# Performance work log

Hardware: AMD Instinct MI355X
Metric: run time of the kernel (lower is better)

## Reference

```python
import jax, jax.numpy as jnp
import numpy as np

# Directable[TL_table[i]] for i = 0..7: (dx, dy) with dx=horizontal shift, dy=vertical shift
# dx=+1 -> shift right (zero-fill col 0), dx=-1 -> shift left; dy=+1 -> shift down, dy=-1 -> shift up.
DIRS = [(1, 1), (0, 1), (-1, 1), (1, 0), (-1, 0), (1, -1), (0, -1), (-1, -1)]


def _shift(img, dx, dy):
    # img: [B, H, W]; zero-padded shift equivalent to bmm with the sparse translation matrices
    if dx == 1:
        img = jnp.pad(img[..., :-1], ((0, 0), (0, 0), (1, 0)))
    elif dx == -1:
        img = jnp.pad(img[..., 1:], ((0, 0), (0, 0), (0, 1)))
    if dy == 1:
        img = jnp.pad(img[:, :-1, :], ((0, 0), (1, 0), (0, 0)))
    elif dy == -1:
        img = jnp.pad(img[:, 1:, :], ((0, 0), (0, 1), (0, 0)))
    return img


def _bce(p, t):
    # torch F.binary_cross_entropy clamps log terms at -100
    logp = jnp.maximum(jnp.log(p), -100.0)
    log1mp = jnp.maximum(jnp.log(1.0 - p), -100.0)
    return -jnp.mean(t * logp + (1.0 - t) * log1mp)


def setup_inputs() -> dict:
    key = jax.random.key(0)
    k1, k2, k3 = jax.random.split(key, 3)
    B, C, H, W = 16, 8, 512, 512
    c_map = jax.random.normal(k1, (B, C, H, W), dtype=jnp.float32)
    target = jax.random.randint(k2, (B, 1, H, W), 0, 2, dtype=jnp.int32)
    con_target = jax.random.randint(k3, (B, C, H, W), 0, 2, dtype=jnp.int32)
    return {"c_map": c_map, "target": target, "con_target": con_target}


def reference(c_map, target, con_target):
    target = target.astype(jnp.float32)        # [B,1,H,W]
    con_target = con_target.astype(jnp.float32)  # [B,8,H,W]

    p = jax.nn.sigmoid(c_map)  # [B,8,H,W]

    # Bilateral voting: shifted[i] = shift(p[:, 7-i]) in direction DIRS[i]
    shifted = jnp.stack(
        [_shift(p[:, 7 - i], dx, dy) for i, (dx, dy) in enumerate(DIRS)], axis=1
    )  # [B,8,H,W]
    vote_out = p * shifted                       # [B,8,H,W] (== bimap.squeeze(1))
    final_pred = jnp.max(vote_out, axis=1, keepdims=True)  # [B,1,H,W]

    # dice loss (sums over dims (1,2) of the 4D tensors, as in the original)
    smooth = 0.001
    i_sum = jnp.sum(target, axis=(1, 2))
    j_sum = jnp.sum(final_pred, axis=(1, 2))
    inter = jnp.sum(target * final_pred, axis=(1, 2))
    loss_dice = jnp.mean(1.0 - (2.0 * inter + smooth) / (i_sum + j_sum + smooth))

    # edge (decouple) loss
    sum_conn = jnp.sum(con_target, axis=1)  # [B,H,W]
    edge = ((sum_conn < 8) & (sum_conn > 0)).astype(p.dtype)
    pred_min = jnp.min(vote_out, axis=1) * edge
    decouple_loss = _bce(pred_min, jnp.zeros_like(pred_min))

    bce_loss = _bce(final_pred, target)
    conmap_l = _bce(p, con_target)
    bimap_l = _bce(vote_out, con_target)

    return 0.8 * conmap_l + decouple_loss + 0.2 * bimap_l + bce_loss + loss_dice
```

## Files before the change

kernel.cpp:

```cpp
#include <hip/hip_runtime.h>

namespace {
constexpr int Bn = 16, Hn = 512, Wn = 512;
constexpr int HW  = Hn * Wn;
constexpr int CHW = 8 * HW;
constexpr int NCOL = Bn * Wn;
constexpr int WALK = 4;
constexpr int GX   = Hn / WALK;
constexpr int NBLK = GX * Bn;
constexpr int SLABN = NBLK * 512;
constexpr int FBLK  = 32;
constexpr int FBLK2 = 256;

constexpr float L2E  = 1.4426950408889634f;
constexpr float LN2  = 0.6931471805599453f;
constexpr float CLMP = -144.26950408889634f;

__device__ __forceinline__ float frcp(float x) { return __builtin_amdgcn_rcpf(x); }
#if __has_builtin(__builtin_amdgcn_exp2f)
__device__ __forceinline__ float fexp2(float x) { return __builtin_amdgcn_exp2f(x); }
#else
__device__ __forceinline__ float fexp2(float x) { return exp2f(x); }
#endif
#if __has_builtin(__builtin_amdgcn_logf)
__device__ __forceinline__ float flog2(float x) { return __builtin_amdgcn_logf(x); }
#else
__device__ __forceinline__ float flog2(float x) { return log2f(x); }
#endif
}


template <bool SLAB>
__global__ __launch_bounds__(256) void bicon_main(
    const float* __restrict__ c_map,
    const int*   __restrict__ target,
    const int*   __restrict__ con_target,
    float* __restrict__ col_i, float* __restrict__ col_j, float* __restrict__ col_x,
    double* __restrict__ bscal)
{
    const int tid  = threadIdx.x;
    const int lane = tid & 63;
    const int wv   = tid >> 6;
    const int b    = blockIdx.y;
    const int hstart = blockIdx.x * WALK;
    const int wq   = wv * 128 + lane * 2;

    const float* cm = c_map      + (size_t)b * CHW;
    const int*   ct = con_target + (size_t)b * CHW;
    const int*   tg = target     + (size_t)b * HW;

    float s_con = 0.f, s_bi = 0.f, s_bce = 0.f, s_dec = 0.f;
    float ci[2] = {0, 0}, cj[2] = {0, 0}, cx[2] = {0, 0};

    auto sig2 = [&](const float2& v, float s[2]) {
        s[0] = frcp(1.f + fexp2(-v.x * L2E));
        s[1] = frcp(1.f + fexp2(-v.y * L2E));
    };

    float C0[2], C1[2], C2[2], P5[2], P6[2], P7[2];
    {
        const int pb = hstart * Wn + wq;
        sig2(*(const float2*)(cm + 0 * HW + pb), C0);
        sig2(*(const float2*)(cm + 1 * HW + pb), C1);
        sig2(*(const float2*)(cm + 2 * HW + pb), C2);
    }
    if (hstart > 0) {
        const int pb = (hstart - 1) * Wn + wq;
        sig2(*(const float2*)(cm + 5 * HW + pb), P5);
        sig2(*(const float2*)(cm + 6 * HW + pb), P6);
        sig2(*(const float2*)(cm + 7 * HW + pb), P7);
    } else {
#pragma unroll
        for (int k = 0; k < 2; ++k) { P5[k] = 0.f; P6[k] = 0.f; P7[k] = 0.f; }
    }

    const bool edR = (wq + 2 == Wn);
    const bool edL = (wq == 0);

    int h = hstart;
#pragma unroll 1
    for (int r = 0; r < WALK; ++r, ++h) {
        const int  base  = h * Wn + wq;
        const bool hasDn = (h + 1 < Hn);
        const bool hasUp = (h > 0);

        const float2 xa3 = *(const float2*)(cm + 3 * HW + base);
        const float2 xa4 = *(const float2*)(cm + 4 * HW + base);
        const float2 xa5 = *(const float2*)(cm + 5 * HW + base);
        const float2 xa6 = *(const float2*)(cm + 6 * HW + base);
        const float2 xa7 = *(const float2*)(cm + 7 * HW + base);
        const float2 xf0 = *(const float2*)(cm + 0 * HW + base + Wn);
        const float2 xf1 = *(const float2*)(cm + 1 * HW + base + Wn);
        const float2 xf2 = *(const float2*)(cm + 2 * HW + base + Wn);
        const float bx0 = cm[0 * HW + base + Wn + 2];
        const float bx2 = cm[2 * HW + base + Wn - 1];
        const float bx3 = cm[3 * HW + base + 2];
        const float bx4 = cm[4 * HW + base - 1];
        const float bx5 = cm[5 * HW + base - Wn + 2];
        const float bx7 = cm[7 * HW + base - Wn - 1];
        const int2  t2  = *(const int2*)(tg + base);

        unsigned lo = 0u;
#pragma unroll
        for (int c = 0; c < 8; ++c) {
            const int2 u = *(const int2*)(ct + c * HW + base);
            lo |= ((unsigned)u.x << c) | ((unsigned)u.y << (8 + c));
        }

        float dp[2] = {1.f, 1.f};
        float ys[2] = {0.f, 0.f};
        float c3[2], c4[2], c5[2], c6[2], c7[2];
        auto fresh = [&](int c, const float2& v, float s[2]) {
            const float xs[2] = {v.x, v.y};
#pragma unroll
            for (int k = 0; k < 2; ++k) {
                const float y = xs[k] * L2E;
                const float e = fexp2(-y);
                const float d = 1.f + e;
                s[k] = frcp(d);
                dp[k] *= d;
                ys[k] += ((lo >> (8 * k + c)) & 1u) ? 0.f : y;
            }
        };
        fresh(3, xa3, c3); fresh(4, xa4, c4); fresh(5, xa5, c5);
        fresh(6, xa6, c6); fresh(7, xa7, c7);

#pragma unroll
        for (int k = 0; k < 2; ++k) {
            const float q0 = ((lo >> (8 * k + 0)) & 1u) ? C0[k] : 1.f - C0[k];
            const float q1 = ((lo >> (8 * k + 1)) & 1u) ? C1[k] : 1.f - C1[k];
            const float q2 = ((lo >> (8 * k + 2)) & 1u) ? C2[k] : 1.f - C2[k];
            s_con += flog2(q0 * q1 * q2) - flog2(dp[k]) - ys[k];
        }

        float F0[2], F1[2], F2[2];
        sig2(xf0, F0); sig2(xf1, F1); sig2(xf2, F2);
        const float s0b = frcp(1.f + fexp2(-bx0 * L2E));
        const float s2b = frcp(1.f + fexp2(-bx2 * L2E));
        const float s3b = frcp(1.f + fexp2(-bx3 * L2E));
        const float s4b = frcp(1.f + fexp2(-bx4 * L2E));
        const float s5b = frcp(1.f + fexp2(-bx5 * L2E));
        const float s7b = frcp(1.f + fexp2(-bx7 * L2E));

        float n0[2], n1[2], n2[2], n3[2], n4[2], n5[2], n6[2], n7[2];
        n0[0] = F0[1]; n3[0] = c3[1]; n5[0] = P5[1];
        n2[1] = F2[0]; n4[1] = c4[0]; n7[1] = P7[0];
        n0[1] = edR ? 0.f : s0b;  n3[1] = edR ? 0.f : s3b;  n5[1] = edR ? 0.f : s5b;
        n2[0] = edL ? 0.f : s2b;  n4[0] = edL ? 0.f : s4b;  n7[0] = edL ? 0.f : s7b;
#pragma unroll
        for (int k = 0; k < 2; ++k) {
            n1[k] = hasDn ? F1[k] : 0.f;
            n6[k] = hasUp ? P6[k] : 0.f;
            if (!hasDn) { n0[k] = 0.f; n2[k] = 0.f; }
            if (!hasUp) { n5[k] = 0.f; n7[k] = 0.f; }
        }

        float vmax[2] = {0.f, 0.f}, vmin[2] = {2.f, 2.f};
        float pr[2]   = {1.f, 1.f};
        float zc[2]   = {0.f, 0.f};
        auto vote = [&](int i, const float p[2], const float n[2]) {
#pragma unroll
            for (int k = 0; k < 2; ++k) {
                const float v = p[k] * n[k];
                vmax[k] = fmaxf(vmax[k], v);
                vmin[k] = fminf(vmin[k], v);
                const bool bit = (lo >> (8 * k + i)) & 1u;
                const bool z   = bit && (v == 0.f);
                float sel = bit ? v : 1.f - v;
                sel = z ? 1.f : sel;
                zc[k] += z ? 1.f : 0.f;
                pr[k] *= sel;
            }
        };
        vote(0, C0, n7); vote(1, C1, n6); vote(2, C2, n5); vote(3, c3, n4);
#pragma unroll
        for (int k = 0; k < 2; ++k) { s_bi += flog2(pr[k]); pr[k] = 1.f; }
        vote(4, c4, n3); vote(5, c5, n2); vote(6, c6, n1); vote(7, c7, n0);
#pragma unroll
        for (int k = 0; k < 2; ++k) { s_bi += flog2(pr[k]) + CLMP * zc[k]; }

        const int tk[2] = {t2.x, t2.y};
#pragma unroll
        for (int k = 0; k < 2; ++k) {
            const float fm = vmax[k];
            s_bce += fmaxf(flog2(tk[k] ? fm : 1.f - fm), CLMP);
            const int sc = __popc((int)((lo >> (8 * k)) & 0xffu));
            s_dec += (sc > 0 && sc < 8) ? fmaxf(flog2(1.f - vmin[k]), CLMP) : 0.f;
            ci[k] += (float)tk[k];
            cj[k] += fm;
            cx[k] += tk[k] ? fm : 0.f;
        }

#pragma unroll
        for (int k = 0; k < 2; ++k) {
            C0[k] = F0[k]; C1[k] = F1[k]; C2[k] = F2[k];
            P5[k] = c5[k]; P6[k] = c6[k]; P7[k] = c7[k];
        }
    }

    if constexpr (SLAB) {
        const size_t sb = ((size_t)(b * GX + blockIdx.x)) << 9;
        float2 vi; vi.x = ci[0]; vi.y = ci[1];
        float2 vj; vj.x = cj[0]; vj.y = cj[1];
        float2 vx; vx.x = cx[0]; vx.y = cx[1];
        *(float2*)(col_i + sb + wq) = vi;
        *(float2*)(col_j + sb + wq) = vj;
        *(float2*)(col_x + sb + wq) = vx;
    } else {
#pragma unroll
        for (int k = 0; k < 2; ++k) {
            atomicAdd(&col_i[b * Wn + wq + k], ci[k]);
            atomicAdd(&col_j[b * Wn + wq + k], cj[k]);
            atomicAdd(&col_x[b * Wn + wq + k], cx[k]);
        }
    }

#pragma unroll
    for (int off = 32; off > 0; off >>= 1) {
        s_con += __shfl_down(s_con, off);
        s_bi  += __shfl_down(s_bi,  off);
        s_bce += __shfl_down(s_bce, off);
        s_dec += __shfl_down(s_dec, off);
    }
    __shared__ float wred[4][4];
    if (lane == 0) {
        wred[wv][0] = s_con * LN2; wred[wv][1] = s_bi * LN2;
        wred[wv][2] = s_bce * LN2; wred[wv][3] = s_dec * LN2;
    }
    __syncthreads();
    if (tid < 4) {
        bscal[((size_t)b * GX + blockIdx.x) * 4 + tid] =
            (double)(wred[0][tid] + wred[1][tid] + wred[2][tid] + wred[3][tid]);
    }
}

__global__ __launch_bounds__(256) void bicon_finish_slab(
    const float* __restrict__ pI,
    const float* __restrict__ pJ,
    const float* __restrict__ pX,
    const double* __restrict__ bscal,
    float* __restrict__ out)
{
    const int tid = threadIdx.x;
    const int w32 = tid & 31;
    const int p   = tid >> 5;
    const int col = blockIdx.x * 32 + w32;
    const int b   = col >> 9;
    const int w   = col & 511;

    float fi = 0.f, fj = 0.f, fx = 0.f;
    const size_t base = (((size_t)(b * GX + p * 16)) << 9) + w;
#pragma unroll
    for (int g = 0; g < 16; ++g) {
        const size_t idx = base + ((size_t)g << 9);
        fi += pI[idx]; fj += pJ[idx]; fx += pX[idx];
    }
    __shared__ float red[3][8][32];
    red[0][p][w32] = fi; red[1][p][w32] = fj; red[2][p][w32] = fx;
    __syncthreads();

    double part = 0.0;
    if (tid < 32) {
        float si = 0.f, sj = 0.f, sx = 0.f;
#pragma unroll
        for (int q = 0; q < 8; ++q) {
            si += red[0][q][tid]; sj += red[1][q][tid]; sx += red[2][q][tid];
        }
        part = (1.0 - (2.0 * (double)sx + 0.001) /
                      ((double)si + (double)sj + 0.001)) / 8192.0;
    }
    if (tid >= 64 && tid < 72) {
        const int s = blockIdx.x * 8 + (tid - 64);
        const double c0 = bscal[s * 4 + 0], c1 = bscal[s * 4 + 1];
        const double c2 = bscal[s * 4 + 2], c3 = bscal[s * 4 + 3];
        part += -0.8 * c0 / 33554432.0 - 0.2 * c1 / 33554432.0
                - c2 / 4194304.0 - c3 / 4194304.0;
    }
#pragma unroll
    for (int off = 32; off > 0; off >>= 1) part += __shfl_down(part, off);
    __shared__ double red2[4];
    if ((tid & 63) == 0) red2[tid >> 6] = part;
    __syncthreads();
    if (tid == 0) atomicAdd(out, (float)(red2[0] + red2[1] + red2[2] + red2[3]));
}

__global__ __launch_bounds__(256) void bicon_finish(
    const float* __restrict__ col_i,
    const float* __restrict__ col_j,
    const float* __restrict__ col_x,
    const double* __restrict__ bscal,
    float* __restrict__ out)
{
    const int tid = threadIdx.x;
    const int col = blockIdx.x * 256 + tid;

    double part;
    {
        const float fi = col_i[col], fj = col_j[col], fx = col_x[col];
        part = (1.0 - (2.0 * (double)fx + 0.001) /
                      ((double)fi + (double)fj + 0.001)) / 8192.0;
    }
    if (tid < 64) {
        const int s = blockIdx.x * 64 + tid;
        const double c0 = bscal[s * 4 + 0], c1 = bscal[s * 4 + 1];
        const double c2 = bscal[s * 4 + 2], c3 = bscal[s * 4 + 3];
        part += -0.8 * c0 / 33554432.0 - 0.2 * c1 / 33554432.0
                - c2 / 4194304.0 - c3 / 4194304.0;
    }
#pragma unroll
    for (int off = 32; off > 0; off >>= 1) part += __shfl_down(part, off);
    __shared__ double red[4];
    if ((tid & 63) == 0) red[tid >> 6] = part;
    __syncthreads();
    if (tid == 0) atomicAdd(out, (float)(red[0] + red[1] + red[2] + red[3]));
}

extern "C" void kernel_launch(void* const* d_in, const int* in_sizes, int n_in,
                              void* d_out, int out_size, void* d_ws, size_t ws_size,
                              hipStream_t stream) {
    const float* c_map      = (const float*)d_in[0];
    const int*   target     = (const int*)d_in[1];
    const int*   con_target = (const int*)d_in[2];
    float* out = (float*)d_out;

    char* ws = (char*)d_ws;
    const size_t slab_need = (size_t)3 * SLABN * sizeof(float)
                           + (size_t)NBLK * 4 * sizeof(double);

    dim3 grid(GX, Bn);
    dim3 block(256);

    hipMemsetAsync(d_out, 0, sizeof(float), stream);

    if (ws_size >= slab_need) {
        float*  pI    = (float*)ws;
        float*  pJ    = pI + SLABN;
        float*  pX    = pJ + SLABN;
        double* bscal = (double*)(ws + (size_t)3 * SLABN * sizeof(float));
        bicon_main<true><<<grid, block, 0, stream>>>(c_map, target, con_target,
                                                     pI, pJ, pX, bscal);
        bicon_finish_slab<<<FBLK2, 256, 0, stream>>>(pI, pJ, pX, bscal, out);
    } else {
        float*  col_i = (float*)ws;
        float*  col_j = col_i + NCOL;
        float*  col_x = col_j + NCOL;
        double* bscal = (double*)(ws + 3 * NCOL * sizeof(float));
        hipMemsetAsync(d_ws, 0, 3 * NCOL * sizeof(float), stream);
        bicon_main<false><<<grid, block, 0, stream>>>(c_map, target, con_target,
                                                      col_i, col_j, col_x, bscal);
        bicon_finish<<<FBLK, 256, 0, stream>>>(col_i, col_j, col_x, bscal, out);
    }
}
```

Measured before the change: 302.4 us.

## Software-prefetch next row's loads and remap block IDs across XCDs

Each loop iteration now issues all global loads for the next row into a register-held struct before computing the current row, and the row loop is fully unrolled, so memory latency overlaps with the sigmoid and log math. Block indices are also permuted so consecutive hardware block IDs (round-robined across the chip's eight XCDs) map to neighbouring work tiles, which is meant to improve L2 locality for the halo rows. The cost is higher register pressure from double-buffering roughly 30 values per thread, which may reduce occupancy.

```diff
diff --git a/kernel.cpp b/kernel.cpp
--- a/kernel.cpp
+++ b/kernel.cpp
@@ -30,6 +30,14 @@
 }
 
 
+struct Row {
+    float2 a3, a4, a5, a6, a7;
+    float2 f0, f1, f2;
+    float  b0, b2, b3, b4, b5, b7;
+    int2   t;
+    int2   u0, u1, u2, u3, u4, u5, u6, u7;
+};
+
 template <bool SLAB>
 __global__ __launch_bounds__(256) void bicon_main(
     const float* __restrict__ c_map,
@@ -41,8 +49,13 @@
     const int tid  = threadIdx.x;
     const int lane = tid & 63;
     const int wv   = tid >> 6;
-    const int b    = blockIdx.y;
-    const int hstart = blockIdx.x * WALK;
+
+    const int hwid = blockIdx.y * GX + blockIdx.x;
+    const int work = (hwid & 7) * (NBLK / 8) + (hwid >> 3);
+    const int gx   = work & (GX - 1);
+    const int b    = work >> 7;
+
+    const int hstart = gx * WALK;
     const int wq   = wv * 128 + lane * 2;
 
     const float* cm = c_map      + (size_t)b * CHW;
@@ -56,6 +69,36 @@
         s[0] = frcp(1.f + fexp2(-v.x * L2E));
         s[1] = frcp(1.f + fexp2(-v.y * L2E));
     };
+
+    auto issue = [&](int hh, Row& R) {
+        const int bs = hh * Wn + wq;
+        R.a3 = *(const float2*)(cm + 3 * HW + bs);
+        R.a4 = *(const float2*)(cm + 4 * HW + bs);
+        R.a5 = *(const float2*)(cm + 5 * HW + bs);
+        R.a6 = *(const float2*)(cm + 6 * HW + bs);
+        R.a7 = *(const float2*)(cm + 7 * HW + bs);
+        R.f0 = *(const float2*)(cm + 0 * HW + bs + Wn);
+        R.f1 = *(const float2*)(cm + 1 * HW + bs + Wn);
+        R.f2 = *(const float2*)(cm + 2 * HW + bs + Wn);
+        R.b0 = cm[0 * HW + bs + Wn + 2];
+        R.b2 = cm[2 * HW + bs + Wn - 1];
+        R.b3 = cm[3 * HW + bs + 2];
+        R.b4 = cm[4 * HW + bs - 1];
+        R.b5 = cm[5 * HW + bs - Wn + 2];
+        R.b7 = cm[7 * HW + bs - Wn - 1];
+        R.t  = *(const int2*)(tg + bs);
+        R.u0 = *(const int2*)(ct + 0 * HW + bs);
+        R.u1 = *(const int2*)(ct + 1 * HW + bs);
+        R.u2 = *(const int2*)(ct + 2 * HW + bs);
+        R.u3 = *(const int2*)(ct + 3 * HW + bs);
+        R.u4 = *(const int2*)(ct + 4 * HW + bs);
+        R.u5 = *(const int2*)(ct + 5 * HW + bs);
+        R.u6 = *(const int2*)(ct + 6 * HW + bs);
+        R.u7 = *(const int2*)(ct + 7 * HW + bs);
+    };
+
+    Row cu, nx;
+    issue(hstart, cu);
 
     float C0[2], C1[2], C2[2], P5[2], P6[2], P7[2];
     {
@@ -77,35 +120,22 @@
     const bool edR = (wq + 2 == Wn);
     const bool edL = (wq == 0);
 
-    int h = hstart;
-#pragma unroll 1
-    for (int r = 0; r < WALK; ++r, ++h) {
+#pragma unroll
+    for (int r = 0; r < WALK; ++r) {
+        const int  h     = hstart + r;
         const int  base  = h * Wn + wq;
         const bool hasDn = (h + 1 < Hn);
         const bool hasUp = (h > 0);
 
-        const float2 xa3 = *(const float2*)(cm + 3 * HW + base);
-        const float2 xa4 = *(const float2*)(cm + 4 * HW + base);
-        const float2 xa5 = *(const float2*)(cm + 5 * HW + base);
-        const float2 xa6 = *(const float2*)(cm + 6 * HW + base);
-        const float2 xa7 = *(const float2*)(cm + 7 * HW + base);
-        const float2 xf0 = *(const float2*)(cm + 0 * HW + base + Wn);
-        const float2 xf1 = *(const float2*)(cm + 1 * HW + base + Wn);
-        const float2 xf2 = *(const float2*)(cm + 2 * HW + base + Wn);
-        const float bx0 = cm[0 * HW + base + Wn + 2];
-        const float bx2 = cm[2 * HW + base + Wn - 1];
-        const float bx3 = cm[3 * HW + base + 2];
-        const float bx4 = cm[4 * HW + base - 1];
-        const float bx5 = cm[5 * HW + base - Wn + 2];
-        const float bx7 = cm[7 * HW + base - Wn - 1];
-        const int2  t2  = *(const int2*)(tg + base);
+        if (r + 1 < WALK) issue(h + 1, nx);
+        (void)base;
 
         unsigned lo = 0u;
-#pragma unroll
-        for (int c = 0; c < 8; ++c) {
-            const int2 u = *(const int2*)(ct + c * HW + base);
+        auto mix = [&](const int2& u, int c) {
             lo |= ((unsigned)u.x << c) | ((unsigned)u.y << (8 + c));
-        }
+        };
+        mix(cu.u0, 0); mix(cu.u1, 1); mix(cu.u2, 2); mix(cu.u3, 3);
+        mix(cu.u4, 4); mix(cu.u5, 5); mix(cu.u6, 6); mix(cu.u7, 7);
 
         float dp[2] = {1.f, 1.f};
         float ys[2] = {0.f, 0.f};
@@ -122,8 +152,8 @@
                 ys[k] += ((lo >> (8 * k + c)) & 1u) ? 0.f : y;
             }
         };
-        fresh(3, xa3, c3); fresh(4, xa4, c4); fresh(5, xa5, c5);
-        fresh(6, xa6, c6); fresh(7, xa7, c7);
+        fresh(3, cu.a3, c3); fresh(4, cu.a4, c4); fresh(5, cu.a5, c5);
+        fresh(6, cu.a6, c6); fresh(7, cu.a7, c7);
 
 #pragma unroll
         for (int k = 0; k < 2; ++k) {
@@ -134,13 +164,13 @@
         }
 
         float F0[2], F1[2], F2[2];
-        sig2(xf0, F0); sig2(xf1, F1); sig2(xf2, F2);
-        const float s0b = frcp(1.f + fexp2(-bx0 * L2E));
-        const float s2b = frcp(1.f + fexp2(-bx2 * L2E));
-        const float s3b = frcp(1.f + fexp2(-bx3 * L2E));
-        const float s4b = frcp(1.f + fexp2(-bx4 * L2E));
-        const float s5b = frcp(1.f + fexp2(-bx5 * L2E));
-        const float s7b = frcp(1.f + fexp2(-bx7 * L2E));
+        sig2(cu.f0, F0); sig2(cu.f1, F1); sig2(cu.f2, F2);
+        const float s0b = frcp(1.f + fexp2(-cu.b0 * L2E));
+        const float s2b = frcp(1.f + fexp2(-cu.b2 * L2E));
+        const float s3b = frcp(1.f + fexp2(-cu.b3 * L2E));
+        const float s4b = frcp(1.f + fexp2(-cu.b4 * L2E));
+        const float s5b = frcp(1.f + fexp2(-cu.b5 * L2E));
+        const float s7b = frcp(1.f + fexp2(-cu.b7 * L2E));
 
         float n0[2], n1[2], n2[2], n3[2], n4[2], n5[2], n6[2], n7[2];
         n0[0] = F0[1]; n3[0] = c3[1]; n5[0] = P5[1];
@@ -179,7 +209,7 @@
 #pragma unroll
         for (int k = 0; k < 2; ++k) { s_bi += flog2(pr[k]) + CLMP * zc[k]; }
 
-        const int tk[2] = {t2.x, t2.y};
+        const int tk[2] = {cu.t.x, cu.t.y};
 #pragma unroll
         for (int k = 0; k < 2; ++k) {
             const float fm = vmax[k];
@@ -196,10 +226,11 @@
             C0[k] = F0[k]; C1[k] = F1[k]; C2[k] = F2[k];
             P5[k] = c5[k]; P6[k] = c6[k]; P7[k] = c7[k];
         }
+        if (r + 1 < WALK) cu = nx;
     }
 
     if constexpr (SLAB) {
-        const size_t sb = ((size_t)(b * GX + blockIdx.x)) << 9;
+        const size_t sb = ((size_t)work) << 9;
         float2 vi; vi.x = ci[0]; vi.y = ci[1];
         float2 vj; vj.x = cj[0]; vj.y = cj[1];
         float2 vx; vx.x = cx[0]; vx.y = cx[1];
@@ -229,7 +260,7 @@
     }
     __syncthreads();
     if (tid < 4) {
-        bscal[((size_t)b * GX + blockIdx.x) * 4 + tid] =
+        bscal[(size_t)work * 4 + tid] =
             (double)(wred[0][tid] + wred[1][tid] + wred[2][tid] + wred[3][tid]);
     }
 }
```

Result: no change. 299.5 us (-1.0%).
